# Performance work log

Measured on AMD Instinct MI355X. Metric: run time of the kernel, lower is better.

## Reference

```python
import jax, jax.numpy as jnp
import numpy as np

B, S, N, F, E, EF, H, L = 4, 16, 2048, 32, 16384, 8, 64, 2
H2 = H // 2


def setup_inputs() -> dict:
    key = jax.random.key(0)
    ks = iter(jax.random.split(key, 40))

    def g(shape, s=0.05):
        return jax.random.normal(next(ks), shape, jnp.float32) * s

    return dict(
        x=jax.random.normal(next(ks), (B, S, N, F), jnp.float32),
        edge_index=jax.random.randint(next(ks), (2, E), 0, N, dtype=jnp.int32),
        edge_attr=jax.random.normal(next(ks), (E, EF), jnp.float32),
        Wp=g((F, H)), bp=jnp.zeros((H,), jnp.float32),
        Wl=g((L, H, H)), bl=jnp.zeros((L, H), jnp.float32),
        Wr=g((L, H, H)), br=jnp.zeros((L, H), jnp.float32),
        We=g((L, EF, H)), att=g((L, H)), gb=jnp.zeros((L, H), jnp.float32),
        Wih=g((L, 3 * H, H)), Whh=g((L, 3 * H, H)),
        bih=jnp.zeros((L, 3 * H), jnp.float32), bhh=jnp.zeros((L, 3 * H), jnp.float32),
        oW1=g((H, H2)), ob1=jnp.zeros((H2,), jnp.float32),
        oW2=g((H2, 1)), ob2=jnp.zeros((1,), jnp.float32),
        dW1=g((H, H2)), db1=jnp.zeros((H2,), jnp.float32),
        dW2=g((H2, 1)), db2=jnp.zeros((1,), jnp.float32),
    )


def reference(x, edge_index, edge_attr, Wp, bp, Wl, bl, Wr, br, We, att, gb,
              Wih, Whh, bih, bhh, oW1, ob1, oW2, ob2, dW1, db1, dW2, db2):
    b, s, n, f = x.shape
    nl, _, h = Wl.shape
    src, dst = edge_index[0], edge_index[1]
    # GATv2Conv add_self_loops with fill_value='mean': self-loop attr = mean of
    # incoming edge attrs per destination node (0 if none).
    ones = jnp.ones((src.shape[0],), x.dtype)
    cnt = jax.ops.segment_sum(ones, dst, num_segments=n)
    loop_attr = jax.ops.segment_sum(edge_attr, dst, num_segments=n) / jnp.maximum(cnt, 1.0)[:, None]
    ar = jnp.arange(n, dtype=src.dtype)
    src_f = jnp.concatenate([src, ar])
    dst_f = jnp.concatenate([dst, ar])
    ea_f = jnp.concatenate([edge_attr, loop_attr], axis=0)  # [E2, EF]

    def gat(Xg, l):
        # Xg: [G, N, H] -- GATv2 (heads=1) applied independently per graph.
        XL = Xg @ Wl[l] + bl[l]
        XR = Xg @ Wr[l] + br[l]
        ep = ea_f @ We[l]                              # [E2, H]
        m = XL[:, src_f] + XR[:, dst_f] + ep[None]     # [G, E2, H]
        m = jax.nn.leaky_relu(m, 0.2)
        logits = m @ att[l]                            # [G, E2]
        seg_max = jax.vmap(lambda lg: jax.ops.segment_max(lg, dst_f, num_segments=n))(logits)
        p = jnp.exp(logits - seg_max[:, dst_f])
        den = jax.vmap(lambda pg: jax.ops.segment_sum(pg, dst_f, num_segments=n))(p)
        alpha = p / den[:, dst_f]
        out = jax.vmap(lambda a, xl: jax.ops.segment_sum(a[:, None] * xl[src_f], dst_f, num_segments=n))(alpha, XL)
        return out + gb[l]

    def gru(seq, l):
        # seq: [T, M, H]; PyTorch GRU gate order (r, z, n), scan over T.
        def step(hprev, xt):
            gi = xt @ Wih[l].T + bih[l]
            gh = hprev @ Whh[l].T + bhh[l]
            ir, iz, inn = jnp.split(gi, 3, -1)
            hr, hz, hn = jnp.split(gh, 3, -1)
            r = jax.nn.sigmoid(ir + hr)
            z = jax.nn.sigmoid(iz + hz)
            nn_ = jnp.tanh(inn + r * hn)
            hnew = (1.0 - z) * nn_ + z * hprev
            return hnew, hnew
        h0 = jnp.zeros(seq.shape[1:], seq.dtype)
        _, ys = jax.lax.scan(step, h0, seq)
        return ys

    X = x @ Wp + bp  # [B, S, N, H]
    for l in range(nl):
        # Original code applies GAT per (outer-t, inner-b) pair; the inner
        # TemporalGNN's GRU recurs over the BATCH axis (length B) per outer t.
        hg = gat(X.reshape(b * s, n, h), l).reshape(b, s, n, h)
        X = gru(hg.reshape(b, s * n, h), l).reshape(b, s, n, h)
    xl = X[:, -1].reshape(b * n, h)  # x[:, -1] then per-node heads, concat dim=1
    order = jax.nn.relu(xl @ oW1 + ob1) @ oW2 + ob2
    demand = jax.nn.relu(xl @ dW1 + db1) @ dW2 + db2
    return order[None], demand[None]  # each [1, B*N, 1]
```

## Files before the change

### kernel.cpp

```cpp
#include <hip/hip_runtime.h>
#include <math.h>

#define Bb   4
#define Ss   16
#define Nn   2048
#define Ff   32
#define Ee   16384
#define EFf  8
#define Hh   64
#define HB2  32
#define E2c  (Ee + Nn)
#define RTOT (Bb*Ss*Nn)
#define Mm   (Ss*Nn)
#define CST  68

typedef __attribute__((ext_vector_type(8))) short short8;
typedef __attribute__((ext_vector_type(4))) float f32x4;
#define MFMA16 __builtin_amdgcn_mfma_f32_16x16x32_bf16

__device__ __forceinline__ float sigf(float x) { return 1.f / (1.f + __expf(-x)); }
__device__ __forceinline__ float tanhfast(float x) { return 2.f / (1.f + __expf(-2.f * x)) - 1.f; }

__device__ __forceinline__ void split_bf16(float x, unsigned short& h, unsigned short& l) {
  unsigned u = __float_as_uint(x);
  unsigned r = (u + 0x7FFFu + ((u >> 16) & 1u)) >> 16;
  h = (unsigned short)r;
  float rest = x - __uint_as_float(r << 16);
  unsigned u2 = __float_as_uint(rest);
  l = (unsigned short)((u2 + 0x7FFFu + ((u2 >> 16) & 1u)) >> 16);
}

template <int PAT>
__device__ __forceinline__ float xorf(float v) {
  return __int_as_float(__builtin_amdgcn_ds_swizzle(__float_as_int(v), PAT));
}
__device__ __forceinline__ float red8(float v) {
  int x = __builtin_amdgcn_update_dpp(0, __float_as_int(v), 0x128, 0xF, 0xF, true);
  v += __int_as_float(x);
  v += xorf<0x401F>(v);
  v += __shfl_xor(v, 32, 64);
  return v;
}
__device__ __forceinline__ float redlogit(float v) {
  int x;
  x = __builtin_amdgcn_update_dpp(0, __float_as_int(v), 0xB1, 0xF, 0xF, true);
  v += __int_as_float(x);
  x = __builtin_amdgcn_update_dpp(0, __float_as_int(v), 0x4E, 0xF, 0xF, true);
  v += __int_as_float(x);
  v += xorf<0x101F>(v);
  return v;
}

__global__ __launch_bounds__(256) void k_loop_accum(
    const int* __restrict__ ei, const float* __restrict__ ea,
    float* __restrict__ cntF, float* __restrict__ loopA) {
  int idx = blockIdx.x * 256 + threadIdx.x;
  int e = idx >> 3, j = idx & 7;
  int d = ei[Ee + e];
  atomicAdd(&loopA[d * EFf + j], ea[idx]);
  if (j == 0) atomicAdd(&cntF[d], 1.0f);
}

__global__ __launch_bounds__(256) void k_scan(
    const float* __restrict__ cntF, int* __restrict__ offs) {
  __shared__ int partial[256];
  int tid = threadIdx.x;
  int base = tid * 8;
  int vals[8];
  int s = 0;
  for (int i = 0; i < 8; ++i) {
    int c = (int)cntF[base + i] + 1;
    vals[i] = c;
    s += c;
  }
  partial[tid] = s;
  __syncthreads();
  for (int off = 1; off < 256; off <<= 1) {
    int v = partial[tid];
    int add = (tid >= off) ? partial[tid - off] : 0;
    __syncthreads();
    partial[tid] = v + add;
    __syncthreads();
  }
  int run = (tid == 0) ? 0 : partial[tid - 1];
  for (int i = 0; i < 8; ++i) {
    offs[base + i] = run;
    run += vals[i];
  }
  if (tid == 255) offs[Nn] = run;
}

__global__ __launch_bounds__(256) void k_scatter(
    const int* __restrict__ ei, const int* __restrict__ offs,
    int* __restrict__ fillI, int* __restrict__ posOf, int* __restrict__ srcA) {
  int e = blockIdx.x * 256 + threadIdx.x;
  if (e >= E2c) return;
  int d = (e < Ee) ? ei[Ee + e] : (e - Ee);
  int s = (e < Ee) ? ei[e]      : (e - Ee);
  int pos = offs[d] + atomicAdd(&fillI[d], 1);
  posOf[e] = pos;
  srcA[pos] = s;
}

__global__ __launch_bounds__(256) void k_wprep(
    const float* __restrict__ Wl, const float* __restrict__ Wr,
    const float* __restrict__ Wih, const float* __restrict__ Whh,
    unsigned short* __restrict__ WXhi, unsigned short* __restrict__ WXlo,
    unsigned short* __restrict__ WGhi, unsigned short* __restrict__ WGlo) {
  int idx = blockIdx.x * 256 + threadIdx.x;
  if (idx < 16384) {
    int j = idx & 7, lane = (idx >> 3) & 63, kh = (idx >> 9) & 1;
    int t = (idx >> 10) & 7, l = idx >> 13;
    int n = t * 16 + (lane & 15);
    int k = kh * 32 + ((lane >> 4) << 3) + j;
    const float* W = (n < 64) ? (Wl + (size_t)l * 4096) : (Wr + (size_t)l * 4096);
    float v = W[k * 64 + (n & 63)];
    unsigned short h, lo;
    split_bf16(v, h, lo);
    WXhi[idx] = h; WXlo[idx] = lo;
  } else {
    int i2 = idx - 16384;
    int j = i2 & 7, lane = (i2 >> 3) & 63, kh = (i2 >> 9) & 1;
    int t = (i2 >> 10) % 24, l = i2 / 24576;
    int n = t * 16 + (lane & 15);
    int k = kh * 32 + ((lane >> 4) << 3) + j;
    int g = n >> 6, c = n & 63;
    const float* W = (g < 3) ? (Wih + (size_t)l * 12288 + (size_t)(g * 64 + c) * 64)
                             : (Whh + (size_t)l * 12288 + (size_t)((g - 3) * 64 + c) * 64);
    float v = W[k];
    unsigned short h, lo;
    split_bf16(v, h, lo);
    WGhi[i2] = h; WGlo[i2] = lo;
  }
}

__global__ __launch_bounds__(256) void k_ep(
    const float* __restrict__ ea, const float* __restrict__ loopA,
    const float* __restrict__ We, const int* __restrict__ posOf,
    const float* __restrict__ cntF, float* __restrict__ EPc) {
  __shared__ float wlds[EFf * Hh];
  int tid = threadIdx.x;
  int l = blockIdx.y;
  const float* Wel = We + (size_t)l * EFf * Hh;
  if (tid < EFf * Hh) wlds[tid] = Wel[tid];
  if (tid + 256 < EFf * Hh) wlds[tid + 256] = Wel[tid + 256];
  __syncthreads();
  int idx = blockIdx.x * 256 + tid;
  int e = idx >> 6, j = idx & 63;
  const float* a = (e < Ee) ? (ea + (size_t)e * EFf) : (loopA + (size_t)(e - Ee) * EFf);
  float acc = 0.f;
#pragma unroll
  for (int k = 0; k < EFf; ++k) acc += a[k] * wlds[k * Hh + j];
  if (e >= Ee) acc /= fmaxf(cntF[e - Ee], 1.0f);
  EPc[(size_t)l * E2c * Hh + (((size_t)posOf[e]) << 6) + j] = acc;
}

__global__ __launch_bounds__(256) void k_proj(
    const float* __restrict__ X, const float* __restrict__ Wp,
    const float* __restrict__ bp, float* __restrict__ Out) {
  __shared__ float w[32 * 16];
  int tid = threadIdx.x;
  int j0 = blockIdx.y << 4;
  for (int idx = tid; idx < 32 * 16; idx += 256)
    w[idx] = Wp[((idx >> 4) << 6) + j0 + (idx & 15)];
  __syncthreads();
  int r0 = (blockIdx.x << 9) + tid;
  float acc[2][16];
#pragma unroll
  for (int jj = 0; jj < 16; ++jj) { float b = bp[j0 + jj]; acc[0][jj] = b; acc[1][jj] = b; }
  const float* x0 = X + ((size_t)r0 << 5);
  const float* x1 = x0 + (256 << 5);
  for (int kc = 0; kc < 8; ++kc) {
    float4 a0 = *(const float4*)(x0 + 4 * kc);
    float4 a1 = *(const float4*)(x1 + 4 * kc);
    float a0a[4] = {a0.x, a0.y, a0.z, a0.w};
    float a1a[4] = {a1.x, a1.y, a1.z, a1.w};
#pragma unroll
    for (int q = 0; q < 4; ++q) {
      const float4* wp4 = (const float4*)(w + ((4 * kc + q) << 4));
#pragma unroll
      for (int q4 = 0; q4 < 4; ++q4) {
        float4 wv = wp4[q4];
        acc[0][4*q4+0] = fmaf(a0a[q], wv.x, acc[0][4*q4+0]);
        acc[0][4*q4+1] = fmaf(a0a[q], wv.y, acc[0][4*q4+1]);
        acc[0][4*q4+2] = fmaf(a0a[q], wv.z, acc[0][4*q4+2]);
        acc[0][4*q4+3] = fmaf(a0a[q], wv.w, acc[0][4*q4+3]);
        acc[1][4*q4+0] = fmaf(a1a[q], wv.x, acc[1][4*q4+0]);
        acc[1][4*q4+1] = fmaf(a1a[q], wv.y, acc[1][4*q4+1]);
        acc[1][4*q4+2] = fmaf(a1a[q], wv.z, acc[1][4*q4+2]);
        acc[1][4*q4+3] = fmaf(a1a[q], wv.w, acc[1][4*q4+3]);
      }
    }
  }
#pragma unroll
  for (int rr = 0; rr < 2; ++rr) {
    float* op = Out + (((size_t)(r0 + 256 * rr)) << 6) + j0;
#pragma unroll
    for (int q4 = 0; q4 < 4; ++q4)
      *(float4*)(op + 4 * q4) = make_float4(acc[rr][4*q4], acc[rr][4*q4+1], acc[rr][4*q4+2], acc[rr][4*q4+3]);
  }
}

__global__ __launch_bounds__(256) void k_xlr_mm(
    const float* __restrict__ X,
    const unsigned short* __restrict__ WXhi, const unsigned short* __restrict__ WXlo,
    const float* __restrict__ bl_, const float* __restrict__ br_,
    float* __restrict__ XL, float* __restrict__ XR) {
  __shared__ unsigned short ahi[4096], alo[4096];
  __shared__ float cbuf[64 * CST];
  int tid = threadIdx.x, lane = tid & 63, wv = tid >> 6;
  size_t m0 = (size_t)blockIdx.x << 6;
#pragma unroll
  for (int it = 0; it < 2; ++it) {
    int task = (it << 8) + tid;
    int row = task >> 3, cOct = task & 7;
    const float* src = X + ((m0 + row) << 6) + (cOct << 3);
    float4 a = *(const float4*)src;
    float4 b = *(const float4*)(src + 4);
    float va[8] = {a.x, a.y, a.z, a.w, b.x, b.y, b.z, b.w};
    short8 hv, lv;
#pragma unroll
    for (int j = 0; j < 8; ++j) {
      unsigned short hs, ls;
      split_bf16(va[j], hs, ls);
      hv[j] = (short)hs; lv[j] = (short)ls;
    }
    int f = ((cOct >> 2) * 4 + (row >> 4)) * 64 + ((cOct & 3) << 4) + (row & 15);
    *(short8*)&ahi[f << 3] = hv;
    *(short8*)&alo[f << 3] = lv;
  }
  __syncthreads();
  short8 Ah0 = *(const short8*)&ahi[((0 + wv) << 6 | lane) << 3];
  short8 Al0 = *(const short8*)&alo[((0 + wv) << 6 | lane) << 3];
  short8 Ah1 = *(const short8*)&ahi[((4 + wv) << 6 | lane) << 3];
  short8 Al1 = *(const short8*)&alo[((4 + wv) << 6 | lane) << 3];
  int nl = lane & 15;
  f32x4 acc[8];
#pragma unroll
  for (int t = 0; t < 8; ++t) {
    int n = t * 16 + nl;
    float b = (n < 64) ? bl_[n] : br_[n - 64];
    acc[t] = (f32x4){b, b, b, b};
  }
#pragma unroll
  for (int t = 0; t < 8; ++t) {
    const short8* bh0p = (const short8*)(WXhi + ((t << 1) << 9)) + lane;
    const short8* bl0p = (const short8*)(WXlo + ((t << 1) << 9)) + lane;
    const short8* bh1p = (const short8*)(WXhi + (((t << 1) + 1) << 9)) + lane;
    const short8* bl1p = (const short8*)(WXlo + (((t << 1) + 1) << 9)) + lane;
    short8 bh0 = *bh0p, bl0 = *bl0p, bh1 = *bh1p, bl1 = *bl1p;
    acc[t] = MFMA16(Ah0, bh0, acc[t], 0, 0, 0);
    acc[t] = MFMA16(Ah0, bl0, acc[t], 0, 0, 0);
    acc[t] = MFMA16(Al0, bh0, acc[t], 0, 0, 0);
    acc[t] = MFMA16(Ah1, bh1, acc[t], 0, 0, 0);
    acc[t] = MFMA16(Ah1, bl1, acc[t], 0, 0, 0);
    acc[t] = MFMA16(Al1, bh1, acc[t], 0, 0, 0);
  }
  int rbase = (wv << 4) + ((lane >> 4) << 2);
#pragma unroll
  for (int half = 0; half < 2; ++half) {
    __syncthreads();
#pragma unroll
    for (int tt = 0; tt < 4; ++tt) {
      int t = (half << 2) + tt;
#pragma unroll
      for (int reg = 0; reg < 4; ++reg)
        cbuf[(rbase + reg) * CST + (tt << 4) + nl] = acc[t][reg];
    }
    __syncthreads();
    float* dst = half ? XR : XL;
#pragma unroll
    for (int i = 0; i < 4; ++i) {
      int idx = (i << 10) + (tid << 2);
      int row = idx >> 6, col = idx & 63;
      *(float4*)(dst + ((m0 + row) << 6) + col) = *(float4*)&cbuf[row * CST + col];
    }
  }
}

__global__ __launch_bounds__(256) void k_gat(
    const float* __restrict__ XL, float* __restrict__ XR_HG,
    const float* __restrict__ EPc, const int* __restrict__ offs,
    const int* __restrict__ srcA,
    const float* __restrict__ att, const float* __restrict__ gbl) {
  int d = blockIdx.x;
  int q = blockIdx.y;
  int tid = threadIdx.x;
  int wv = tid >> 6, lane = tid & 63;
  int eSub = lane >> 3, hOct = lane & 7;
  int hb = hOct << 3;
  float at[8], gv[8];
  {
    float4 a0 = *(const float4*)(att + hb);
    float4 a1 = *(const float4*)(att + hb + 4);
    float4 g0v = *(const float4*)(gbl + hb);
    float4 g1v = *(const float4*)(gbl + hb + 4);
    at[0]=a0.x; at[1]=a0.y; at[2]=a0.z; at[3]=a0.w;
    at[4]=a1.x; at[5]=a1.y; at[6]=a1.z; at[7]=a1.w;
    gv[0]=g0v.x; gv[1]=g0v.y; gv[2]=g0v.z; gv[3]=g0v.w;
    gv[4]=g1v.x; gv[5]=g1v.y; gv[6]=g1v.z; gv[7]=g1v.w;
  }
  int p0 = offs[d], p1 = offs[d + 1];
  int nE = p1 - p0;
  int nCh = (nE + 7) >> 3;
  int gbase = (q << 4) + wv;
  size_t rowg[4];
  const float* Xg[4];
  float xr[4][8];
#pragma unroll
  for (int c = 0; c < 4; ++c) {
    int g = gbase + (c << 2);
    rowg[c] = ((size_t)(g * Nn + d)) << 6;
    Xg[c] = XL + (((size_t)g * Nn) << 6);
    float4 a = *(const float4*)(XR_HG + rowg[c] + hb);
    float4 b = *(const float4*)(XR_HG + rowg[c] + hb + 4);
    xr[c][0]=a.x; xr[c][1]=a.y; xr[c][2]=a.z; xr[c][3]=a.w;
    xr[c][4]=b.x; xr[c][5]=b.y; xr[c][6]=b.z; xr[c][7]=b.w;
  }
  float Sd[4] = {0.f, 0.f, 0.f, 0.f};
  float acc[4][8];
#pragma unroll
  for (int c = 0; c < 4; ++c)
#pragma unroll
    for (int j = 0; j < 8; ++j) acc[c][j] = 0.f;

  for (int ck = 0; ck < nCh; ++ck) {
    int p = (ck << 3) + eSub;
    int pc = p < nE ? p : nE - 1;
    int s = srcA[p0 + pc];
    const float* epp = EPc + (((size_t)(p0 + pc)) << 6) + hb;
    float4 e0 = *(const float4*)epp;
    float4 e1 = *(const float4*)(epp + 4);
    float ep[8] = {e0.x, e0.y, e0.z, e0.w, e1.x, e1.y, e1.z, e1.w};
    float xlv[4][8];
#pragma unroll
    for (int c = 0; c < 4; ++c) {
      const float* xp = Xg[c] + ((size_t)s << 6) + hb;
      float4 x0 = *(const float4*)xp;
      float4 x1 = *(const float4*)(xp + 4);
      xlv[c][0]=x0.x; xlv[c][1]=x0.y; xlv[c][2]=x0.z; xlv[c][3]=x0.w;
      xlv[c][4]=x1.x; xlv[c][5]=x1.y; xlv[c][6]=x1.z; xlv[c][7]=x1.w;
    }
    float v[4] = {0.f, 0.f, 0.f, 0.f};
#pragma unroll
    for (int c = 0; c < 4; ++c)
#pragma unroll
      for (int j = 0; j < 8; ++j) {
        float m = xlv[c][j] + xr[c][j] + ep[j];
        m = fmaxf(m, 0.2f * m);
        v[c] = fmaf(m, at[j], v[c]);
      }
#pragma unroll
    for (int c = 0; c < 4; ++c) v[c] = redlogit(v[c]);
    bool live = (p < nE);
#pragma unroll
    for (int c = 0; c < 4; ++c) {
      float w = live ? __expf(v[c]) : 0.f;
      Sd[c] += w;
#pragma unroll
      for (int j = 0; j < 8; ++j) acc[c][j] = fmaf(w, xlv[c][j], acc[c][j]);
    }
  }
#pragma unroll
  for (int c = 0; c < 4; ++c) {
    Sd[c] = red8(Sd[c]);
#pragma unroll
    for (int j = 0; j < 8; ++j) acc[c][j] = red8(acc[c][j]);
  }
  if (eSub == 0) {
#pragma unroll
    for (int c = 0; c < 4; ++c) {
      float inv = 1.f / Sd[c];
      float* op = XR_HG + rowg[c] + hb;
      *(float4*)(op)     = make_float4(fmaf(acc[c][0], inv, gv[0]), fmaf(acc[c][1], inv, gv[1]),
                                       fmaf(acc[c][2], inv, gv[2]), fmaf(acc[c][3], inv, gv[3]));
      *(float4*)(op + 4) = make_float4(fmaf(acc[c][4], inv, gv[4]), fmaf(acc[c][5], inv, gv[5]),
                                       fmaf(acc[c][6], inv, gv[6]), fmaf(acc[c][7], inv, gv[7]));
    }
  }
}

__device__ __forceinline__ void mm6r(f32x4& acc,
    short8 Ah0, short8 Al0, short8 Ah1, short8 Al1,
    short8 bh0, short8 bl0, short8 bh1, short8 bl1) {
  acc = MFMA16(Ah0, bh0, acc, 0, 0, 0);
  acc = MFMA16(Ah0, bl0, acc, 0, 0, 0);
  acc = MFMA16(Al0, bh0, acc, 0, 0, 0);
  acc = MFMA16(Ah1, bh1, acc, 0, 0, 0);
  acc = MFMA16(Ah1, bl1, acc, 0, 0, 0);
  acc = MFMA16(Al1, bh1, acc, 0, 0, 0);
}

__global__ __launch_bounds__(256, 2) void k_gru_fused(
    const float* __restrict__ hgAll,
    const unsigned short* __restrict__ WGhi, const unsigned short* __restrict__ WGlo,
    const float* __restrict__ bih, const float* __restrict__ bhh,
    float* __restrict__ houtAll) {
  __shared__ unsigned short ghi[4096], glo[4096];
  __shared__ float cbuf[64 * CST];
  int tid = threadIdx.x, lane = tid & 63, wv = tid >> 6;
  int nl = lane & 15;
  int rb0 = (lane >> 4) << 2;
  size_t m0 = (size_t)blockIdx.x << 6;

  short8 Wh[6][2], Wl[6][2];
#pragma unroll
  for (int g = 0; g < 6; ++g) {
    int tt = wv + (g << 2);
    Wh[g][0] = *((const short8*)(WGhi + (tt << 10)) + lane);
    Wh[g][1] = *((const short8*)(WGhi + (tt << 10) + 512) + lane);
    Wl[g][0] = *((const short8*)(WGlo + (tt << 10)) + lane);
    Wl[g][1] = *((const short8*)(WGlo + (tt << 10) + 512) + lane);
  }

  float biasR, biasZ, biasN, biasH;
  {
    int c = (wv << 4) + nl;
    biasR = bih[c]       + bhh[c];
    biasZ = bih[64 + c]  + bhh[64 + c];
    biasN = bih[128 + c];
    biasH = bhh[128 + c];
  }

  float4 pa[2], pb[2];
#pragma unroll
  for (int it = 0; it < 2; ++it) {
    int task = (it << 8) + tid;
    int row = task >> 3, cOct = task & 7;
    const float* srcg = hgAll + ((m0 + row) << 6) + (cOct << 3);
    pa[it] = *(const float4*)srcg;
    pb[it] = *(const float4*)(srcg + 4);
  }

  for (int t = 0; t < Bb; ++t) {
#pragma unroll
    for (int it = 0; it < 2; ++it) {
      int task = (it << 8) + tid;
      int row = task >> 3, cOct = task & 7;
      float va[8] = {pa[it].x, pa[it].y, pa[it].z, pa[it].w,
                     pb[it].x, pb[it].y, pb[it].z, pb[it].w};
      short8 hv8, lv8;
#pragma unroll
      for (int j = 0; j < 8; ++j) {
        unsigned short hs, ls;
        split_bf16(va[j], hs, ls);
        hv8[j] = (short)hs; lv8[j] = (short)ls;
      }
      int f = ((cOct >> 2) * 4 + (row >> 4)) * 64 + ((cOct & 3) << 4) + (row & 15);
      *(short8*)&ghi[f << 3] = hv8;
      *(short8*)&glo[f << 3] = lv8;
    }
    __syncthreads();

    if (t + 1 < Bb) {
      const float* hg = hgAll + (size_t)(t + 1) * ((size_t)Mm * Hh);
#pragma unroll
      for (int it = 0; it < 2; ++it) {
        int task = (it << 8) + tid;
        int row = task >> 3, cOct = task & 7;
        const float* srcg = hg + ((m0 + row) << 6) + (cOct << 3);
        pa[it] = *(const float4*)srcg;
        pb[it] = *(const float4*)(srcg + 4);
      }
    }

    f32x4 accR[4], accZ[4], accN[4], accH[4];
#pragma unroll
    for (int rg = 0; rg < 4; ++rg) {
      accR[rg] = (f32x4){biasR, biasR, biasR, biasR};
      accZ[rg] = (f32x4){biasZ, biasZ, biasZ, biasZ};
      accN[rg] = (f32x4){biasN, biasN, biasN, biasN};
      accH[rg] = (f32x4){biasH, biasH, biasH, biasH};
    }
#pragma unroll
    for (int rg = 0; rg < 4; ++rg) {
      short8 Gh0 = *(const short8*)&ghi[((0 + rg) << 6 | lane) << 3];
      short8 Gl0 = *(const short8*)&glo[((0 + rg) << 6 | lane) << 3];
      short8 Gh1 = *(const short8*)&ghi[((4 + rg) << 6 | lane) << 3];
      short8 Gl1 = *(const short8*)&glo[((4 + rg) << 6 | lane) << 3];
      mm6r(accR[rg], Gh0, Gl0, Gh1, Gl1, Wh[0][0], Wl[0][0], Wh[0][1], Wl[0][1]);
      mm6r(accZ[rg], Gh0, Gl0, Gh1, Gl1, Wh[1][0], Wl[1][0], Wh[1][1], Wl[1][1]);
      mm6r(accN[rg], Gh0, Gl0, Gh1, Gl1, Wh[2][0], Wl[2][0], Wh[2][1], Wl[2][1]);
      if (t) {
        const float* cb = &cbuf[((rg << 4) + (lane & 15)) * CST + ((lane >> 4) << 3)];
        float4 p00 = *(const float4*)cb;
        float4 p01 = *(const float4*)(cb + 4);
        float4 p10 = *(const float4*)(cb + 32);
        float4 p11 = *(const float4*)(cb + 36);
        float v0[8] = {p00.x, p00.y, p00.z, p00.w, p01.x, p01.y, p01.z, p01.w};
        float v1[8] = {p10.x, p10.y, p10.z, p10.w, p11.x, p11.y, p11.z, p11.w};
        short8 Ph0, Pl0, Ph1, Pl1;
#pragma unroll
        for (int j = 0; j < 8; ++j) {
          unsigned short hs, ls;
          split_bf16(v0[j], hs, ls);
          Ph0[j] = (short)hs; Pl0[j] = (short)ls;
          split_bf16(v1[j], hs, ls);
          Ph1[j] = (short)hs; Pl1[j] = (short)ls;
        }
        mm6r(accR[rg], Ph0, Pl0, Ph1, Pl1, Wh[3][0], Wl[3][0], Wh[3][1], Wl[3][1]);
        mm6r(accZ[rg], Ph0, Pl0, Ph1, Pl1, Wh[4][0], Wl[4][0], Wh[4][1], Wl[4][1]);
        mm6r(accH[rg], Ph0, Pl0, Ph1, Pl1, Wh[5][0], Wl[5][0], Wh[5][1], Wl[5][1]);
      }
    }
    __syncthreads();

#pragma unroll
    for (int rg = 0; rg < 4; ++rg) {
#pragma unroll
      for (int r = 0; r < 4; ++r) {
        float rgate = sigf(accR[rg][r]);
        float zg = sigf(accZ[rg][r]);
        float ng = tanhfast(accN[rg][r] + rgate * accH[rg][r]);
        int ci = ((rg << 4) + rb0 + r) * CST + (wv << 4) + nl;
        float hp = t ? cbuf[ci] : 0.f;
        cbuf[ci] = (1.f - zg) * ng + zg * hp;
      }
    }
    __syncthreads();

    float* hout = houtAll + (size_t)t * ((size_t)Mm * Hh);
#pragma unroll
    for (int i = 0; i < 4; ++i) {
      int idx = (i << 10) + (tid << 2);
      int row = idx >> 6, col = idx & 63;
      *(float4*)(hout + ((m0 + row) << 6) + col) = *(float4*)&cbuf[row * CST + col];
    }
  }
}

__global__ __launch_bounds__(256) void k_heads(
    const float* __restrict__ Xb,
    const float* __restrict__ oW1, const float* __restrict__ ob1,
    const float* __restrict__ oW2, const float* __restrict__ ob2,
    const float* __restrict__ dW1, const float* __restrict__ db1,
    const float* __restrict__ dW2, const float* __restrict__ db2,
    float* __restrict__ out) {
  __shared__ float xa[64 * 65];
  __shared__ float w1o[64 * 32], w1d[64 * 32];
  __shared__ float po[4][64], pd[4][64];
  int tid = threadIdx.x;
  int rblk = blockIdx.x << 6;
  int b = rblk >> 11;
  int n0 = rblk & (Nn - 1);
  const float* src = Xb + (((size_t)b * Ss + (Ss - 1)) * Nn + n0) * Hh;
#pragma unroll
  for (int i = 0; i < 4; ++i) {
    int idx = (i << 10) + (tid << 2);
    int row = idx >> 6, col = idx & 63;
    float4 v = *(const float4*)(src + idx);
    float* dp = &xa[row * 65 + col];
    dp[0] = v.x; dp[1] = v.y; dp[2] = v.z; dp[3] = v.w;
  }
  for (int idx = tid; idx < 2048; idx += 256) {
    w1o[idx] = oW1[idx];
    w1d[idx] = dW1[idx];
  }
  __syncthreads();
  int row = tid & 63;
  int jg = tid >> 6;
  int j0 = jg << 3;
  float hO[8], hD[8];
#pragma unroll
  for (int j = 0; j < 8; ++j) { hO[j] = ob1[j0 + j]; hD[j] = db1[j0 + j]; }
  const float* xr = &xa[row * 65];
  for (int k = 0; k < 64; ++k) {
    float xv = xr[k];
    const float4* wo = (const float4*)&w1o[(k << 5) + j0];
    const float4* wd = (const float4*)&w1d[(k << 5) + j0];
    float4 o0 = wo[0], o1 = wo[1], d0 = wd[0], d1 = wd[1];
    hO[0] = fmaf(xv, o0.x, hO[0]); hO[1] = fmaf(xv, o0.y, hO[1]);
    hO[2] = fmaf(xv, o0.z, hO[2]); hO[3] = fmaf(xv, o0.w, hO[3]);
    hO[4] = fmaf(xv, o1.x, hO[4]); hO[5] = fmaf(xv, o1.y, hO[5]);
    hO[6] = fmaf(xv, o1.z, hO[6]); hO[7] = fmaf(xv, o1.w, hO[7]);
    hD[0] = fmaf(xv, d0.x, hD[0]); hD[1] = fmaf(xv, d0.y, hD[1]);
    hD[2] = fmaf(xv, d0.z, hD[2]); hD[3] = fmaf(xv, d0.w, hD[3]);
    hD[4] = fmaf(xv, d1.x, hD[4]); hD[5] = fmaf(xv, d1.y, hD[5]);
    hD[6] = fmaf(xv, d1.z, hD[6]); hD[7] = fmaf(xv, d1.w, hD[7]);
  }
  float accoP = 0.f, accdP = 0.f;
#pragma unroll
  for (int j = 0; j < 8; ++j) {
    accoP = fmaf(fmaxf(hO[j], 0.f), oW2[j0 + j], accoP);
    accdP = fmaf(fmaxf(hD[j], 0.f), dW2[j0 + j], accdP);
  }
  po[jg][row] = accoP;
  pd[jg][row] = accdP;
  __syncthreads();
  if (tid < 64) {
    int r = rblk + tid;
    out[r]           = ob2[0] + ((po[0][tid] + po[1][tid]) + (po[2][tid] + po[3][tid]));
    out[Bb * Nn + r] = db2[0] + ((pd[0][tid] + pd[1][tid]) + (pd[2][tid] + pd[3][tid]));
  }
}

extern "C" void kernel_launch(void* const* d_in, const int* in_sizes, int n_in,
                              void* d_out, int out_size, void* d_ws, size_t ws_size,
                              hipStream_t stream) {
  const float* x   = (const float*)d_in[0];
  const int*   ei  = (const int*)d_in[1];
  const float* ea  = (const float*)d_in[2];
  const float* Wp  = (const float*)d_in[3];
  const float* bp  = (const float*)d_in[4];
  const float* Wl  = (const float*)d_in[5];
  const float* bl  = (const float*)d_in[6];
  const float* Wr  = (const float*)d_in[7];
  const float* br  = (const float*)d_in[8];
  const float* We  = (const float*)d_in[9];
  const float* att = (const float*)d_in[10];
  const float* gb  = (const float*)d_in[11];
  const float* Wih = (const float*)d_in[12];
  const float* Whh = (const float*)d_in[13];
  const float* bih = (const float*)d_in[14];
  const float* bhh = (const float*)d_in[15];
  const float* oW1 = (const float*)d_in[16];
  const float* ob1 = (const float*)d_in[17];
  const float* oW2 = (const float*)d_in[18];
  const float* ob2 = (const float*)d_in[19];
  const float* dW1 = (const float*)d_in[20];
  const float* db1 = (const float*)d_in[21];
  const float* dW2 = (const float*)d_in[22];
  const float* db2 = (const float*)d_in[23];
  float* out = (float*)d_out;

  float* f    = (float*)d_ws;
  float* Xb   = f;
  float* XLb  = Xb  + (size_t)RTOT * Hh;
  float* XRb  = XLb + (size_t)RTOT * Hh;
  float* EPc  = XRb + (size_t)RTOT * Hh;
  unsigned short* WXhi = (unsigned short*)(EPc + (size_t)2 * E2c * Hh);
  unsigned short* WXlo = WXhi + 16384;
  unsigned short* WGhi = WXlo + 16384;
  unsigned short* WGlo = WGhi + 49152;
  float* cntF = (float*)(WGlo + 49152);
  float* loopA = cntF + Nn;
  int*   fillI = (int*)(loopA + Nn * EFf);
  int*   offs  = fillI + Nn;
  int*   posOf = offs + 2052;
  int*   srcA  = posOf + E2c;

  hipMemsetAsync(cntF, 0, (size_t)(Nn + Nn * EFf + Nn) * 4, stream);

  k_loop_accum<<<dim3(Ee * EFf / 256), 256, 0, stream>>>(ei, ea, cntF, loopA);
  k_scan<<<1, 256, 0, stream>>>(cntF, offs);
  k_scatter<<<dim3((E2c + 255) / 256), 256, 0, stream>>>(ei, offs, fillI, posOf, srcA);
  k_wprep<<<dim3(256), 256, 0, stream>>>(Wl, Wr, Wih, Whh, WXhi, WXlo, WGhi, WGlo);

  k_proj<<<dim3(RTOT / 512, 4), 256, 0, stream>>>(x, Wp, bp, Xb);

  k_ep<<<dim3(E2c * Hh / 256, 2), 256, 0, stream>>>(ea, loopA, We, posOf, cntF, EPc);

  for (int l = 0; l < 2; ++l) {
    k_xlr_mm<<<dim3(RTOT / 64), 256, 0, stream>>>(
        Xb, WXhi + (size_t)l * 8192, WXlo + (size_t)l * 8192,
        bl + (size_t)l * Hh, br + (size_t)l * Hh, XLb, XRb);
    k_gat<<<dim3(Nn, 4), 256, 0, stream>>>(
        XLb, XRb, EPc + (size_t)l * E2c * Hh, offs, srcA,
        att + (size_t)l * Hh, gb + (size_t)l * Hh);
    k_gru_fused<<<dim3(Mm / 64), 256, 0, stream>>>(
        XRb, WGhi + (size_t)l * 24576, WGlo + (size_t)l * 24576,
        bih + (size_t)l * 192, bhh + (size_t)l * 192, Xb);
  }

  k_heads<<<dim3(Bb * Nn / 64), 256, 0, stream>>>(
      Xb, oW1, ob1, oW2, ob2, dW1, db1, dW2, db2, out);
}
```

Baseline: 375.9 us.

## Store XL node-major across graphs and linearize GAT grid for gather locality

The projection kernel now writes XL transposed to a [node][graph][H] layout, so all 64 graphs' features for one source node are contiguous. The GAT kernel gathers XL rows for a source node across its graph slice from one contiguous 16 KB region instead of 64 scattered rows. The GAT grid is flattened so the four graph-quarter blocks of the same destination node get adjacent block IDs and can share cached source rows. The cost is strided scattered stores in the projection epilogue.

```diff
diff --git a/kernel.cpp b/kernel.cpp
--- a/kernel.cpp
+++ b/kernel.cpp
@@ -268,12 +268,23 @@
         cbuf[(rbase + reg) * CST + (tt << 4) + nl] = acc[t][reg];
     }
     __syncthreads();
-    float* dst = half ? XR : XL;
-#pragma unroll
-    for (int i = 0; i < 4; ++i) {
-      int idx = (i << 10) + (tid << 2);
-      int row = idx >> 6, col = idx & 63;
-      *(float4*)(dst + ((m0 + row) << 6) + col) = *(float4*)&cbuf[row * CST + col];
+    if (half == 0) {
+      int g = (int)(m0 >> 11);
+      int nodeBase = (int)(m0 & 2047);
+#pragma unroll
+      for (int i = 0; i < 4; ++i) {
+        int idx = (i << 10) + (tid << 2);
+        int row = idx >> 6, col = idx & 63;
+        size_t off = ((((size_t)(nodeBase + row)) << 6) + g) << 6;
+        *(float4*)(XL + off + col) = *(float4*)&cbuf[row * CST + col];
+      }
+    } else {
+#pragma unroll
+      for (int i = 0; i < 4; ++i) {
+        int idx = (i << 10) + (tid << 2);
+        int row = idx >> 6, col = idx & 63;
+        *(float4*)(XR + ((m0 + row) << 6) + col) = *(float4*)&cbuf[row * CST + col];
+      }
     }
   }
 }
@@ -283,8 +294,9 @@
     const float* __restrict__ EPc, const int* __restrict__ offs,
     const int* __restrict__ srcA,
     const float* __restrict__ att, const float* __restrict__ gbl) {
-  int d = blockIdx.x;
-  int q = blockIdx.y;
+  int bid = blockIdx.x;
+  int d = bid >> 2;
+  int q = bid & 3;
   int tid = threadIdx.x;
   int wv = tid >> 6, lane = tid & 63;
   int eSub = lane >> 3, hOct = lane & 7;
@@ -305,13 +317,11 @@
   int nCh = (nE + 7) >> 3;
   int gbase = (q << 4) + wv;
   size_t rowg[4];
-  const float* Xg[4];
   float xr[4][8];
 #pragma unroll
   for (int c = 0; c < 4; ++c) {
     int g = gbase + (c << 2);
     rowg[c] = ((size_t)(g * Nn + d)) << 6;
-    Xg[c] = XL + (((size_t)g * Nn) << 6);
     float4 a = *(const float4*)(XR_HG + rowg[c] + hb);
     float4 b = *(const float4*)(XR_HG + rowg[c] + hb + 4);
     xr[c][0]=a.x; xr[c][1]=a.y; xr[c][2]=a.z; xr[c][3]=a.w;
@@ -332,12 +342,12 @@
     float4 e0 = *(const float4*)epp;
     float4 e1 = *(const float4*)(epp + 4);
     float ep[8] = {e0.x, e0.y, e0.z, e0.w, e1.x, e1.y, e1.z, e1.w};
+    const float* xb = XL + (((size_t)s) << 12) + (gbase << 6) + hb;
     float xlv[4][8];
 #pragma unroll
     for (int c = 0; c < 4; ++c) {
-      const float* xp = Xg[c] + ((size_t)s << 6) + hb;
-      float4 x0 = *(const float4*)xp;
-      float4 x1 = *(const float4*)(xp + 4);
+      float4 x0 = *(const float4*)(xb + (c << 8));
+      float4 x1 = *(const float4*)(xb + (c << 8) + 4);
       xlv[c][0]=x0.x; xlv[c][1]=x0.y; xlv[c][2]=x0.z; xlv[c][3]=x0.w;
       xlv[c][4]=x1.x; xlv[c][5]=x1.y; xlv[c][6]=x1.z; xlv[c][7]=x1.w;
     }
@@ -654,7 +664,7 @@
     k_xlr_mm<<<dim3(RTOT / 64), 256, 0, stream>>>(
         Xb, WXhi + (size_t)l * 8192, WXlo + (size_t)l * 8192,
         bl + (size_t)l * Hh, br + (size_t)l * Hh, XLb, XRb);
-    k_gat<<<dim3(Nn, 4), 256, 0, stream>>>(
+    k_gat<<<dim3(Nn * 4), 256, 0, stream>>>(
         XLb, XRb, EPc + (size_t)l * E2c * Hh, offs, srcA,
         att + (size_t)l * Hh, gb + (size_t)l * Hh);
     k_gru_fused<<<dim3(Mm / 64), 256, 0, stream>>>(
```

Result: slower. 408.7 us (+8.7%).
